# Kernel tuning notes

Hardware: AMD Instinct MI355X
Metric: run time of the kernel (lower is better)

## Reference

```python
import jax, jax.numpy as jnp
import numpy as np

N_NODES = 100000
N_EDGES = 1600000
D = 128
L = 4          # GIN layers
H = 32         # inner MLP hidden width (hard-coded in create_mlp)
BN_EPS = 1e-5


def setup_inputs() -> dict:
    key = jax.random.key(0)
    ks = jax.random.split(key, 8)
    X = jax.random.normal(ks[0], (N_NODES, D), dtype=jnp.float32)
    edge_index = jax.random.randint(ks[1], (2, N_EDGES), 0, N_NODES, dtype=jnp.int64)
    eps = jax.random.normal(ks[2], (L,), dtype=jnp.float32)
    W1 = jax.random.normal(ks[3], (L, H, D), dtype=jnp.float32) * 0.1
    W2 = jax.random.normal(ks[4], (L, H, H), dtype=jnp.float32) * 0.1
    W3 = jax.random.normal(ks[5], (L, D, H), dtype=jnp.float32) * 0.1
    return {
        "X": X, "edge_index": edge_index, "eps": eps,
        "W1": W1, "b1": jnp.zeros((L, H), jnp.float32),
        "g1": jnp.ones((L, H), jnp.float32), "bt1": jnp.zeros((L, H), jnp.float32),
        "W2": W2, "b2": jnp.zeros((L, H), jnp.float32),
        "g2": jnp.ones((L, H), jnp.float32), "bt2": jnp.zeros((L, H), jnp.float32),
        "W3": W3, "b3": jnp.zeros((L, D), jnp.float32),
    }


def _bn(x, g, b):
    # BatchNorm1d in training mode: biased batch stats over the node axis
    m = jnp.mean(x, axis=0)
    v = jnp.var(x, axis=0)
    return g * (x - m) * jax.lax.rsqrt(v + BN_EPS) + b


def reference(X, edge_index, eps, W1, b1, g1, bt1, W2, b2, g2, bt2, W3, b3):
    src, dst = edge_index[0], edge_index[1]
    for l in range(L):
        # identity-message scatter-add neighbor aggregation
        S = jax.ops.segment_sum(X[src], dst, num_segments=N_NODES)  # [N, D_l]
        Z = (1.0 + eps[l]) * X + S
        # inner MLP: Lin->BN->ReLU, Lin->BN->ReLU, Lin
        h = jax.nn.relu(_bn(Z @ W1[l].T + b1[l], g1[l], bt1[l]))
        h = jax.nn.relu(_bn(h @ W2[l].T + b2[l], g2[l], bt2[l]))
        X = h @ W3[l].T + b3[l]
    return X
```

## Files before the change

### kernel.cpp

```cpp
#include <hip/hip_runtime.h>

#define NN 100000
#define NE 1600000
#define DD 128
#define HH 32
#define NB 196
#define SB 256
#define EPB 6250
#define BCAP 12288

#define OFF_P        0UL
#define OFF_T        12800000UL
#define OFF_PK       25600000UL
#define OFF_ROWOFF   32000000UL
#define OFF_COUNTS   32400128UL
#define OFF_POFS     32600832UL
#define OFF_BTOT     32801536UL
#define OFF_BBASE    32802560UL
#define OFF_STATS    32803584UL
#define OFF_W1T      32819968UL
#define OFF_W2T      32836352UL
#define OFF_MT       32852736UL
#define OFF_C        32865024UL
#define OFF_W3T      32865536UL

__global__ void __launch_bounds__(256) k_count(const int* __restrict__ ei,
                                               int* __restrict__ counts) {
    __shared__ int c[NB];
    int t = threadIdx.x;
    if (t < NB) c[t] = 0;
    __syncthreads();
    int s = blockIdx.x * EPB;
    for (int e = s + t; e < s + EPB; e += 256)
        atomicAdd(&c[ei[NE + e] >> 9], 1);
    __syncthreads();
    if (t < NB) counts[t * SB + blockIdx.x] = c[t];
}

__global__ void __launch_bounds__(256) k_scanX(const int* __restrict__ counts,
                                               int* __restrict__ pofs,
                                               int* __restrict__ btot) {
    __shared__ int s[256];
    int t = threadIdx.x, b = blockIdx.x;
    int v = counts[b * SB + t];
    s[t] = v;
    __syncthreads();
    for (int off = 1; off < 256; off <<= 1) {
        int x = (t >= off) ? s[t - off] : 0;
        __syncthreads();
        s[t] += x;
        __syncthreads();
    }
    pofs[b * SB + t] = s[t] - v;
    if (t == 255) btot[b] = s[255];
}

__global__ void __launch_bounds__(256) k_scanY(const int* __restrict__ btot,
                                               int* __restrict__ bbase,
                                               int* __restrict__ row_off) {
    __shared__ int s[256];
    int t = threadIdx.x;
    int v = (t < NB) ? btot[t] : 0;
    s[t] = v;
    __syncthreads();
    for (int off = 1; off < 256; off <<= 1) {
        int x = (t >= off) ? s[t - off] : 0;
        __syncthreads();
        s[t] += x;
        __syncthreads();
    }
    if (t < NB) bbase[t] = s[t] - v;
    if (t == NB - 1) bbase[NB] = s[t];
    if (t == 0) row_off[NN] = NE;
}

__global__ void __launch_bounds__(256) k_scatter(const int* __restrict__ ei,
                                                 const int* __restrict__ pofs,
                                                 const int* __restrict__ bbase,
                                                 int* __restrict__ pk) {
    __shared__ int cur[NB];
    int t = threadIdx.x, blk = blockIdx.x;
    if (t < NB) cur[t] = bbase[t] + pofs[t * SB + blk];
    __syncthreads();
    int s = blk * EPB;
    for (int e = s + t; e < s + EPB; e += 256) {
        int src = ei[e], dst = ei[NE + e];
        int b = dst >> 9;
        int pos = atomicAdd(&cur[b], 1);
        pk[pos] = (src << 9) | (dst & 511);
    }
}

__global__ void __launch_bounds__(256) k_bucket(int* pk,
                                                const int* __restrict__ bbase,
                                                int* __restrict__ row_off) {
    __shared__ int cnt[512];
    __shared__ int ts[256];
    __shared__ int stage[BCAP];
    int t = threadIdx.x, b = blockIdx.x;
    int base = bbase[b], end = bbase[b + 1];
    cnt[t] = 0; cnt[t + 256] = 0;
    __syncthreads();
    for (int e = base + t; e < end; e += 256)
        atomicAdd(&cnt[pk[e] & 511], 1);
    __syncthreads();
    int a0 = cnt[2 * t], a1 = cnt[2 * t + 1];
    int p = a0 + a1;
    ts[t] = p;
    __syncthreads();
    for (int off = 1; off < 256; off <<= 1) {
        int x = (t >= off) ? ts[t - off] : 0;
        __syncthreads();
        ts[t] += x;
        __syncthreads();
    }
    int ex = ts[t] - p;
    cnt[2 * t] = ex;
    cnt[2 * t + 1] = ex + a0;
    int n0 = b * 512 + 2 * t;
    if (n0 < NN)     row_off[n0]     = base + ex;
    if (n0 + 1 < NN) row_off[n0 + 1] = base + ex + a0;
    __syncthreads();
    for (int e = base + t; e < end; e += 256) {
        int v = pk[e];
        int pos = atomicAdd(&cnt[v & 511], 1);
        stage[pos] = v >> 9;
    }
    __syncthreads();
    int sz = end - base;
    for (int i = t; i < sz; i += 256) pk[base + i] = stage[i];
}

__global__ void __launch_bounds__(256) k_prep(const float* __restrict__ W1,
                                              const float* __restrict__ W2,
                                              const float* __restrict__ W3,
                                              const float* __restrict__ b3,
                                              float* __restrict__ W1T,
                                              float* __restrict__ W2T,
                                              float* __restrict__ MT,
                                              float* __restrict__ C,
                                              float* __restrict__ W3T) {
    int t = threadIdx.x, b = blockIdx.x;
    if (b < 12) {
        int d = b * 256 + t;
        int l = d >> 10, rem = d & 1023;
        int i = rem >> 5, j = rem & 31;
        const float* w1r = W1 + (l + 1) * HH * DD + i * DD;
        const float* w3c = W3 + l * DD * HH + j;
        float m = 0.f;
#pragma unroll 8
        for (int k = 0; k < DD; k++) m += w1r[k] * w3c[k * HH];
        MT[l * 1024 + j * 32 + i] = m;
    } else if (b == 12) {
        for (int idx = t; idx < 4096; idx += 256) {
            int jj = idx >> 7, kk = idx & 127;
            W1T[kk * 32 + jj] = W1[jj * 128 + kk];
        }
    } else if (b == 13) {
        for (int idx = t; idx < 4096; idx += 256) {
            int l = idx >> 10, rem = idx & 1023;
            int i = rem >> 5, j = rem & 31;
            W2T[l * 1024 + j * 32 + i] = W2[l * 1024 + i * 32 + j];
        }
    } else if (b == 14) {
        for (int idx = t; idx < 4096; idx += 256) {
            int jj = idx >> 5, kk = idx & 31;
            W3T[kk * 128 + jj] = W3[3 * 4096 + jj * 32 + kk];
        }
    } else {
        if (t < 96) {
            int l = t >> 5, ii = t & 31;
            const float* w1r = W1 + (l + 1) * HH * DD + ii * DD;
            const float* bb = b3 + l * DD;
            float c = 0.f;
#pragma unroll 8
            for (int k = 0; k < DD; k++) c += w1r[k] * bb[k];
            C[l * 32 + ii] = c;
        }
    }
}

__global__ void __launch_bounds__(256) k_P(const float4* __restrict__ X4,
                                           const float4* __restrict__ W1T4,
                                           float4* __restrict__ P4) {
    __shared__ float xs[128 * 33];
    int t = threadIdx.x, blk = blockIdx.x;
    int i = t & 7, g = t >> 3;
    int nbase = blk * 128;
    float4 acc[4];
#pragma unroll
    for (int j = 0; j < 4; j++) acc[j] = make_float4(0.f, 0.f, 0.f, 0.f);
    for (int kt = 0; kt < 4; kt++) {
        __syncthreads();
#pragma unroll
        for (int q = 0; q < 4; q++) {
            int idx = t + 256 * q;
            int nd = idx >> 3, c4 = idx & 7;
            int node = nbase + nd;
            if (node > NN - 1) node = NN - 1;
            float4 v = X4[(size_t)node * 32 + kt * 8 + c4];
            float* dst = xs + nd * 33 + 4 * c4;
            dst[0] = v.x; dst[1] = v.y; dst[2] = v.z; dst[3] = v.w;
        }
        __syncthreads();
        const float4* Wk = W1T4 + (size_t)(kt * 32) * 8 + i;
        const float* xr0 = xs + (g * 4) * 33;
#pragma unroll
        for (int k = 0; k < 32; k++) {
            float4 w = Wk[k * 8];
            float x0 = xr0[k], x1 = xr0[33 + k], x2 = xr0[66 + k], x3 = xr0[99 + k];
            acc[0].x += x0 * w.x; acc[0].y += x0 * w.y; acc[0].z += x0 * w.z; acc[0].w += x0 * w.w;
            acc[1].x += x1 * w.x; acc[1].y += x1 * w.y; acc[1].z += x1 * w.z; acc[1].w += x1 * w.w;
            acc[2].x += x2 * w.x; acc[2].y += x2 * w.y; acc[2].z += x2 * w.z; acc[2].w += x2 * w.w;
            acc[3].x += x3 * w.x; acc[3].y += x3 * w.y; acc[3].z += x3 * w.z; acc[3].w += x3 * w.w;
        }
    }
    int node = nbase + g * 4;
#pragma unroll
    for (int j = 0; j < 4; j++)
        if (node + j < NN) P4[(size_t)(node + j) * 8 + i] = acc[j];
}

__global__ void __launch_bounds__(256) k_A(const float4* __restrict__ P4,
                                           const int* __restrict__ csr,
                                           const int* __restrict__ row_off,
                                           const float* __restrict__ eps,
                                           const float* __restrict__ b1, int l,
                                           float4* __restrict__ T4,
                                           float* __restrict__ gs) {
    __shared__ float ls[64];
    int t = threadIdx.x;
    if (t < 64) ls[t] = 0.f;
    __syncthreads();
    int g = t >> 3, i = t & 7;
    int n = blockIdx.x * 32 + g;
    float e1 = 1.f + eps[l];
    int e0 = row_off[n], eend = row_off[n + 1];
    float4 p = P4[(size_t)n * 8 + i];
    float4 acc;
    acc.x = e1 * p.x; acc.y = e1 * p.y; acc.z = e1 * p.z; acc.w = e1 * p.w;
    int e = e0;
    for (; e + 4 <= eend; e += 4) {
        int s0 = csr[e], s1 = csr[e + 1], s2 = csr[e + 2], s3 = csr[e + 3];
        float4 q0 = P4[(size_t)s0 * 8 + i];
        float4 q1 = P4[(size_t)s1 * 8 + i];
        float4 q2 = P4[(size_t)s2 * 8 + i];
        float4 q3 = P4[(size_t)s3 * 8 + i];
        acc.x += (q0.x + q1.x) + (q2.x + q3.x);
        acc.y += (q0.y + q1.y) + (q2.y + q3.y);
        acc.z += (q0.z + q1.z) + (q2.z + q3.z);
        acc.w += (q0.w + q1.w) + (q2.w + q3.w);
    }
    for (; e < eend; e++) {
        int s = csr[e];
        float4 q = P4[(size_t)s * 8 + i];
        acc.x += q.x; acc.y += q.y; acc.z += q.z; acc.w += q.w;
    }
    float4 bb = ((const float4*)(b1 + l * 32))[i];
    acc.x += bb.x; acc.y += bb.y; acc.z += bb.z; acc.w += bb.w;
    T4[(size_t)n * 8 + i] = acc;
    float sx = acc.x, sy = acc.y, sz = acc.z, sw = acc.w;
    float qx = acc.x * acc.x, qy = acc.y * acc.y, qz = acc.z * acc.z, qw = acc.w * acc.w;
#pragma unroll
    for (int off = 8; off < 64; off <<= 1) {
        sx += __shfl_xor(sx, off); sy += __shfl_xor(sy, off);
        sz += __shfl_xor(sz, off); sw += __shfl_xor(sw, off);
        qx += __shfl_xor(qx, off); qy += __shfl_xor(qy, off);
        qz += __shfl_xor(qz, off); qw += __shfl_xor(qw, off);
    }
    if ((t & 56) == 0) {
        atomicAdd(&ls[4 * i + 0], sx); atomicAdd(&ls[4 * i + 1], sy);
        atomicAdd(&ls[4 * i + 2], sz); atomicAdd(&ls[4 * i + 3], sw);
        atomicAdd(&ls[32 + 4 * i + 0], qx); atomicAdd(&ls[32 + 4 * i + 1], qy);
        atomicAdd(&ls[32 + 4 * i + 2], qz); atomicAdd(&ls[32 + 4 * i + 3], qw);
    }
    __syncthreads();
    if (t < 64) atomicAdd(&gs[(blockIdx.x & 7) * 64 + t], ls[t]);
}

__global__ void __launch_bounds__(256) k_D(float4* __restrict__ T4,
                                           const float4* __restrict__ W2T4,
                                           const float* __restrict__ b2,
                                           const float* __restrict__ g1,
                                           const float* __restrict__ bt1, int l,
                                           float* __restrict__ gs) {
    __shared__ float sc[32], sh[32], ls[64], a1s[128 * 33];
    int t = threadIdx.x, blk = blockIdx.x;
    if (t < 32) {
        float s0 = 0.f, s1 = 0.f;
#pragma unroll
        for (int r = 0; r < 8; r++) { s0 += gs[r * 64 + t]; s1 += gs[r * 64 + 32 + t]; }
        float m = s0 * (1.f / NN);
        float var = s1 * (1.f / NN) - m * m;
        float s = g1[l * 32 + t] * rsqrtf(var + 1e-5f);
        sc[t] = s; sh[t] = bt1[l * 32 + t] - m * s;
    } else if (t >= 64 && t < 128) {
        ls[t - 64] = 0.f;
    }
    __syncthreads();
    int nbase = blk * 128;
#pragma unroll
    for (int q = 0; q < 4; q++) {
        int idx = t + 256 * q;
        int nd = idx >> 3, c4 = idx & 7;
        int node = nbase + nd;
        if (node > NN - 1) node = NN - 1;
        float4 x = T4[(size_t)node * 8 + c4];
        float* dst = a1s + nd * 33 + 4 * c4;
        dst[0] = fmaxf(x.x * sc[4 * c4 + 0] + sh[4 * c4 + 0], 0.f);
        dst[1] = fmaxf(x.y * sc[4 * c4 + 1] + sh[4 * c4 + 1], 0.f);
        dst[2] = fmaxf(x.z * sc[4 * c4 + 2] + sh[4 * c4 + 2], 0.f);
        dst[3] = fmaxf(x.w * sc[4 * c4 + 3] + sh[4 * c4 + 3], 0.f);
    }
    __syncthreads();
    int i = t & 7, g = t >> 3;
    const float4* b24 = (const float4*)(b2 + l * 32);
    float4 b = b24[i];
    float4 acc[4];
#pragma unroll
    for (int j = 0; j < 4; j++) acc[j] = b;
    const float* xr0 = a1s + (g * 4) * 33;
#pragma unroll
    for (int k = 0; k < 32; k++) {
        float4 w = W2T4[k * 8 + i];
        float x0 = xr0[k], x1 = xr0[33 + k], x2 = xr0[66 + k], x3 = xr0[99 + k];
        acc[0].x += x0 * w.x; acc[0].y += x0 * w.y; acc[0].z += x0 * w.z; acc[0].w += x0 * w.w;
        acc[1].x += x1 * w.x; acc[1].y += x1 * w.y; acc[1].z += x1 * w.z; acc[1].w += x1 * w.w;
        acc[2].x += x2 * w.x; acc[2].y += x2 * w.y; acc[2].z += x2 * w.z; acc[2].w += x2 * w.w;
        acc[3].x += x3 * w.x; acc[3].y += x3 * w.y; acc[3].z += x3 * w.z; acc[3].w += x3 * w.w;
    }
    int node = nbase + g * 4;
    float sx = 0.f, sy = 0.f, sz = 0.f, sw = 0.f;
    float qx = 0.f, qy = 0.f, qz = 0.f, qw = 0.f;
#pragma unroll
    for (int j = 0; j < 4; j++) {
        if (node + j < NN) {
            T4[(size_t)(node + j) * 8 + i] = acc[j];
            sx += acc[j].x; sy += acc[j].y; sz += acc[j].z; sw += acc[j].w;
            qx += acc[j].x * acc[j].x; qy += acc[j].y * acc[j].y;
            qz += acc[j].z * acc[j].z; qw += acc[j].w * acc[j].w;
        }
    }
#pragma unroll
    for (int off = 8; off < 64; off <<= 1) {
        sx += __shfl_xor(sx, off); sy += __shfl_xor(sy, off);
        sz += __shfl_xor(sz, off); sw += __shfl_xor(sw, off);
        qx += __shfl_xor(qx, off); qy += __shfl_xor(qy, off);
        qz += __shfl_xor(qz, off); qw += __shfl_xor(qw, off);
    }
    if ((t & 56) == 0) {
        atomicAdd(&ls[4 * i + 0], sx); atomicAdd(&ls[4 * i + 1], sy);
        atomicAdd(&ls[4 * i + 2], sz); atomicAdd(&ls[4 * i + 3], sw);
        atomicAdd(&ls[32 + 4 * i + 0], qx); atomicAdd(&ls[32 + 4 * i + 1], qy);
        atomicAdd(&ls[32 + 4 * i + 2], qz); atomicAdd(&ls[32 + 4 * i + 3], qw);
    }
    __syncthreads();
    if (t < 64) atomicAdd(&gs[512 + (blk & 7) * 64 + t], ls[t]);
}

__global__ void __launch_bounds__(256) k_Fm(const float4* __restrict__ T4,
                                            const float* __restrict__ g2,
                                            const float* __restrict__ bt2, int l,
                                            const float* __restrict__ gs,
                                            const float4* __restrict__ MT4,
                                            const float* __restrict__ C,
                                            float4* __restrict__ P4) {
    __shared__ float sc[32], sh[32], a2s[128 * 33];
    int t = threadIdx.x, blk = blockIdx.x;
    if (t < 32) {
        float s0 = 0.f, s1 = 0.f;
#pragma unroll
        for (int r = 0; r < 8; r++) { s0 += gs[512 + r * 64 + t]; s1 += gs[512 + r * 64 + 32 + t]; }
        float m = s0 * (1.f / NN);
        float var = s1 * (1.f / NN) - m * m;
        float s = g2[l * 32 + t] * rsqrtf(var + 1e-5f);
        sc[t] = s; sh[t] = bt2[l * 32 + t] - m * s;
    }
    __syncthreads();
    int nbase = blk * 128;
#pragma unroll
    for (int q = 0; q < 4; q++) {
        int idx = t + 256 * q;
        int nd = idx >> 3, c4 = idx & 7;
        int node = nbase + nd;
        if (node > NN - 1) node = NN - 1;
        float4 x = T4[(size_t)node * 8 + c4];
        float* dst = a2s + nd * 33 + 4 * c4;
        dst[0] = fmaxf(x.x * sc[4 * c4 + 0] + sh[4 * c4 + 0], 0.f);
        dst[1] = fmaxf(x.y * sc[4 * c4 + 1] + sh[4 * c4 + 1], 0.f);
        dst[2] = fmaxf(x.z * sc[4 * c4 + 2] + sh[4 * c4 + 2], 0.f);
        dst[3] = fmaxf(x.w * sc[4 * c4 + 3] + sh[4 * c4 + 3], 0.f);
    }
    __syncthreads();
    int i = t & 7, g = t >> 3;
    const float4* C4 = (const float4*)(C + l * 32);
    float4 c0 = C4[i];
    float4 acc[4];
#pragma unroll
    for (int j = 0; j < 4; j++) acc[j] = c0;
    const float* xr0 = a2s + (g * 4) * 33;
    const float4* Mt = MT4 + l * 256;
#pragma unroll
    for (int k = 0; k < 32; k++) {
        float4 w = Mt[k * 8 + i];
        float x0 = xr0[k], x1 = xr0[33 + k], x2 = xr0[66 + k], x3 = xr0[99 + k];
        acc[0].x += x0 * w.x; acc[0].y += x0 * w.y; acc[0].z += x0 * w.z; acc[0].w += x0 * w.w;
        acc[1].x += x1 * w.x; acc[1].y += x1 * w.y; acc[1].z += x1 * w.z; acc[1].w += x1 * w.w;
        acc[2].x += x2 * w.x; acc[2].y += x2 * w.y; acc[2].z += x2 * w.z; acc[2].w += x2 * w.w;
        acc[3].x += x3 * w.x; acc[3].y += x3 * w.y; acc[3].z += x3 * w.z; acc[3].w += x3 * w.w;
    }
    int node = nbase + g * 4;
#pragma unroll
    for (int j = 0; j < 4; j++)
        if (node + j < NN) P4[(size_t)(node + j) * 8 + i] = acc[j];
}

__global__ void __launch_bounds__(256) k_F3(const float4* __restrict__ T4,
                                            const float* __restrict__ g2,
                                            const float* __restrict__ bt2,
                                            const float* __restrict__ gs,
                                            const float4* __restrict__ W3T4,
                                            const float* __restrict__ b3,
                                            float4* __restrict__ out4) {
    __shared__ float sc[32], sh[32], a2s[32 * 33];
    int t = threadIdx.x, blk = blockIdx.x;
    if (t < 32) {
        float s0 = 0.f, s1 = 0.f;
#pragma unroll
        for (int r = 0; r < 8; r++) { s0 += gs[512 + r * 64 + t]; s1 += gs[512 + r * 64 + 32 + t]; }
        float m = s0 * (1.f / NN);
        float var = s1 * (1.f / NN) - m * m;
        float s = g2[3 * 32 + t] * rsqrtf(var + 1e-5f);
        sc[t] = s; sh[t] = bt2[3 * 32 + t] - m * s;
    }
    __syncthreads();
    {
        int nd = t >> 3, c4 = t & 7;
        float4 x = T4[(size_t)(blk * 32 + nd) * 8 + c4];
        float* dst = a2s + nd * 33 + 4 * c4;
        dst[0] = fmaxf(x.x * sc[4 * c4 + 0] + sh[4 * c4 + 0], 0.f);
        dst[1] = fmaxf(x.y * sc[4 * c4 + 1] + sh[4 * c4 + 1], 0.f);
        dst[2] = fmaxf(x.z * sc[4 * c4 + 2] + sh[4 * c4 + 2], 0.f);
        dst[3] = fmaxf(x.w * sc[4 * c4 + 3] + sh[4 * c4 + 3], 0.f);
    }
    __syncthreads();
    int j = t & 31, g = t >> 5;
    const float4* b34 = (const float4*)(b3 + 3 * 128);
    float4 b = b34[j];
    float4 acc[4];
#pragma unroll
    for (int jj = 0; jj < 4; jj++) acc[jj] = b;
    const float* xr0 = a2s + (g * 4) * 33;
#pragma unroll
    for (int k = 0; k < 32; k++) {
        float4 w = W3T4[k * 32 + j];
        float x0 = xr0[k], x1 = xr0[33 + k], x2 = xr0[66 + k], x3 = xr0[99 + k];
        acc[0].x += x0 * w.x; acc[0].y += x0 * w.y; acc[0].z += x0 * w.z; acc[0].w += x0 * w.w;
        acc[1].x += x1 * w.x; acc[1].y += x1 * w.y; acc[1].z += x1 * w.z; acc[1].w += x1 * w.w;
        acc[2].x += x2 * w.x; acc[2].y += x2 * w.y; acc[2].z += x2 * w.z; acc[2].w += x2 * w.w;
        acc[3].x += x3 * w.x; acc[3].y += x3 * w.y; acc[3].z += x3 * w.z; acc[3].w += x3 * w.w;
    }
    size_t node = (size_t)blk * 32 + g * 4;
#pragma unroll
    for (int jj = 0; jj < 4; jj++)
        out4[(node + jj) * 32 + j] = acc[jj];
}

extern "C" void kernel_launch(void* const* d_in, const int* in_sizes, int n_in,
                              void* d_out, int out_size, void* d_ws, size_t ws_size,
                              hipStream_t stream) {
    const float* X   = (const float*)d_in[0];
    const int*   EI  = (const int*)d_in[1];
    const float* eps = (const float*)d_in[2];
    const float* W1  = (const float*)d_in[3];
    const float* b1  = (const float*)d_in[4];
    const float* g1  = (const float*)d_in[5];
    const float* bt1 = (const float*)d_in[6];
    const float* W2  = (const float*)d_in[7];
    const float* b2  = (const float*)d_in[8];
    const float* g2  = (const float*)d_in[9];
    const float* bt2 = (const float*)d_in[10];
    const float* W3  = (const float*)d_in[11];
    const float* b3  = (const float*)d_in[12];

    char* ws = (char*)d_ws;
    float* P       = (float*)(ws + OFF_P);
    float* T       = (float*)(ws + OFF_T);
    int*   pk      = (int*)(ws + OFF_PK);
    int*   row_off = (int*)(ws + OFF_ROWOFF);
    int*   counts  = (int*)(ws + OFF_COUNTS);
    int*   pofs    = (int*)(ws + OFF_POFS);
    int*   btot    = (int*)(ws + OFF_BTOT);
    int*   bbase   = (int*)(ws + OFF_BBASE);
    float* stats   = (float*)(ws + OFF_STATS);
    float* W1T     = (float*)(ws + OFF_W1T);
    float* W2T     = (float*)(ws + OFF_W2T);
    float* MT      = (float*)(ws + OFF_MT);
    float* C       = (float*)(ws + OFF_C);
    float* W3T     = (float*)(ws + OFF_W3T);

    hipMemsetAsync(ws + OFF_STATS, 0, 16384, stream);

    k_count<<<SB, 256, 0, stream>>>(EI, counts);
    k_prep<<<16, 256, 0, stream>>>(W1, W2, W3, b3, W1T, W2T, MT, C, W3T);
    k_scanX<<<NB, 256, 0, stream>>>(counts, pofs, btot);
    k_scanY<<<1, 256, 0, stream>>>(btot, bbase, row_off);
    k_scatter<<<SB, 256, 0, stream>>>(EI, pofs, bbase, pk);
    k_bucket<<<NB, 256, 0, stream>>>(pk, bbase, row_off);
    k_P<<<782, 256, 0, stream>>>((const float4*)X, (const float4*)W1T, (float4*)P);

    for (int l = 0; l < 4; l++) {
        float* gs = stats + l * 1024;
        k_A<<<NN / 32, 256, 0, stream>>>((const float4*)P, pk, row_off, eps, b1, l,
                                         (float4*)T, gs);
        k_D<<<782, 256, 0, stream>>>((float4*)T,
                                     (const float4*)(W2T + (size_t)l * 1024),
                                     b2, g1, bt1, l, gs);
        if (l < 3)
            k_Fm<<<782, 256, 0, stream>>>((const float4*)T, g2, bt2, l, gs,
                                          (const float4*)MT, C, (float4*)P);
        else
            k_F3<<<3125, 256, 0, stream>>>((const float4*)T, g2, bt2, gs,
                                           (const float4*)W3T, b3, (float4*)d_out);
    }
}
```

Before: 475.2 us.

## Partition CSR edges by source quarter and gather per quarter for locality

Each node's incoming edges are now sorted into four source-index ranges, with a 4×N offset table replacing row_off. The aggregation kernel has each block handle 128 nodes and walks the quarters in sequence, so gathers from all blocks running at once tend to hit the same 3.2 MB slice of P and stay in cache. The costs are fewer, larger blocks with more registers each, a bigger offset table, and more histogram bins in the bucket kernel.

After: 554.0 us. +16.6%, slower.

```diff
diff --git a/kernel.cpp b/kernel.cpp
--- a/kernel.cpp
+++ b/kernel.cpp
@@ -8,21 +8,26 @@
 #define SB 256
 #define EPB 6250
 #define BCAP 12288
+#define QS 25000
 
 #define OFF_P        0UL
 #define OFF_T        12800000UL
 #define OFF_PK       25600000UL
-#define OFF_ROWOFF   32000000UL
-#define OFF_COUNTS   32400128UL
-#define OFF_POFS     32600832UL
-#define OFF_BTOT     32801536UL
-#define OFF_BBASE    32802560UL
-#define OFF_STATS    32803584UL
-#define OFF_W1T      32819968UL
-#define OFF_W2T      32836352UL
-#define OFF_MT       32852736UL
-#define OFF_C        32865024UL
-#define OFF_W3T      32865536UL
+#define OFF_QOFF     32000000UL
+#define OFF_COUNTS   33600128UL
+#define OFF_POFS     33800832UL
+#define OFF_BTOT     34001536UL
+#define OFF_BBASE    34002560UL
+#define OFF_STATS    34003584UL
+#define OFF_W1T      34019968UL
+#define OFF_W2T      34036352UL
+#define OFF_MT       34052736UL
+#define OFF_C        34065024UL
+#define OFF_W3T      34065536UL
+
+__device__ __forceinline__ int src_quad(int s) {
+    return (s >= 2 * QS) ? ((s >= 3 * QS) ? 3 : 2) : ((s >= QS) ? 1 : 0);
+}
 
 __global__ void __launch_bounds__(256) k_count(const int* __restrict__ ei,
                                                int* __restrict__ counts) {
@@ -57,7 +62,7 @@
 
 __global__ void __launch_bounds__(256) k_scanY(const int* __restrict__ btot,
                                                int* __restrict__ bbase,
-                                               int* __restrict__ row_off) {
+                                               int* __restrict__ qoff) {
     __shared__ int s[256];
     int t = threadIdx.x;
     int v = (t < NB) ? btot[t] : 0;
@@ -71,7 +76,7 @@
     }
     if (t < NB) bbase[t] = s[t] - v;
     if (t == NB - 1) bbase[NB] = s[t];
-    if (t == 0) row_off[NN] = NE;
+    if (t == 0) qoff[4 * NN] = NE;
 }
 
 __global__ void __launch_bounds__(256) k_scatter(const int* __restrict__ ei,
@@ -93,19 +98,24 @@
 
 __global__ void __launch_bounds__(256) k_bucket(int* pk,
                                                 const int* __restrict__ bbase,
-                                                int* __restrict__ row_off) {
-    __shared__ int cnt[512];
+                                                int* __restrict__ qoff) {
+    __shared__ int cnt[2048];
     __shared__ int ts[256];
     __shared__ int stage[BCAP];
     int t = threadIdx.x, b = blockIdx.x;
     int base = bbase[b], end = bbase[b + 1];
-    cnt[t] = 0; cnt[t + 256] = 0;
-    __syncthreads();
-    for (int e = base + t; e < end; e += 256)
-        atomicAdd(&cnt[pk[e] & 511], 1);
-    __syncthreads();
-    int a0 = cnt[2 * t], a1 = cnt[2 * t + 1];
-    int p = a0 + a1;
+#pragma unroll
+    for (int j = 0; j < 8; j++) cnt[t * 8 + j] = 0;
+    __syncthreads();
+    for (int e = base + t; e < end; e += 256) {
+        int v = pk[e];
+        atomicAdd(&cnt[((v & 511) << 2) | src_quad(v >> 9)], 1);
+    }
+    __syncthreads();
+    int c8[8];
+    int p = 0;
+#pragma unroll
+    for (int j = 0; j < 8; j++) { c8[j] = cnt[t * 8 + j]; p += c8[j]; }
     ts[t] = p;
     __syncthreads();
     for (int off = 1; off < 256; off <<= 1) {
@@ -114,17 +124,21 @@
         ts[t] += x;
         __syncthreads();
     }
-    int ex = ts[t] - p;
-    cnt[2 * t] = ex;
-    cnt[2 * t + 1] = ex + a0;
-    int n0 = b * 512 + 2 * t;
-    if (n0 < NN)     row_off[n0]     = base + ex;
-    if (n0 + 1 < NN) row_off[n0 + 1] = base + ex + a0;
+    int run = ts[t] - p;
+#pragma unroll
+    for (int j = 0; j < 8; j++) {
+        int ci = t * 8 + j;
+        cnt[ci] = run;
+        int n0 = b * 512 + (ci >> 2);
+        if (n0 < NN) qoff[n0 * 4 + (ci & 3)] = base + run;
+        run += c8[j];
+    }
     __syncthreads();
     for (int e = base + t; e < end; e += 256) {
         int v = pk[e];
-        int pos = atomicAdd(&cnt[v & 511], 1);
-        stage[pos] = v >> 9;
+        int src = v >> 9;
+        int pos = atomicAdd(&cnt[((v & 511) << 2) | src_quad(src)], 1);
+        stage[pos] = src;
     }
     __syncthreads();
     int sz = end - base;
@@ -223,7 +237,7 @@
 
 __global__ void __launch_bounds__(256) k_A(const float4* __restrict__ P4,
                                            const int* __restrict__ csr,
-                                           const int* __restrict__ row_off,
+                                           const int* __restrict__ qoff,
                                            const float* __restrict__ eps,
                                            const float* __restrict__ b1, int l,
                                            float4* __restrict__ T4,
@@ -231,36 +245,60 @@
     __shared__ float ls[64];
     int t = threadIdx.x;
     if (t < 64) ls[t] = 0.f;
-    __syncthreads();
     int g = t >> 3, i = t & 7;
-    int n = blockIdx.x * 32 + g;
+    int nbase = blockIdx.x * 128;
     float e1 = 1.f + eps[l];
-    int e0 = row_off[n], eend = row_off[n + 1];
-    float4 p = P4[(size_t)n * 8 + i];
-    float4 acc;
-    acc.x = e1 * p.x; acc.y = e1 * p.y; acc.z = e1 * p.z; acc.w = e1 * p.w;
-    int e = e0;
-    for (; e + 4 <= eend; e += 4) {
-        int s0 = csr[e], s1 = csr[e + 1], s2 = csr[e + 2], s3 = csr[e + 3];
-        float4 q0 = P4[(size_t)s0 * 8 + i];
-        float4 q1 = P4[(size_t)s1 * 8 + i];
-        float4 q2 = P4[(size_t)s2 * 8 + i];
-        float4 q3 = P4[(size_t)s3 * 8 + i];
-        acc.x += (q0.x + q1.x) + (q2.x + q3.x);
-        acc.y += (q0.y + q1.y) + (q2.y + q3.y);
-        acc.z += (q0.z + q1.z) + (q2.z + q3.z);
-        acc.w += (q0.w + q1.w) + (q2.w + q3.w);
-    }
-    for (; e < eend; e++) {
-        int s = csr[e];
-        float4 q = P4[(size_t)s * 8 + i];
-        acc.x += q.x; acc.y += q.y; acc.z += q.z; acc.w += q.w;
+    float4 acc[4];
+#pragma unroll
+    for (int p = 0; p < 4; p++) {
+        int n = nbase + p * 32 + g;
+        if (n < NN) {
+            float4 x = P4[(size_t)n * 8 + i];
+            acc[p].x = e1 * x.x; acc[p].y = e1 * x.y;
+            acc[p].z = e1 * x.z; acc[p].w = e1 * x.w;
+        } else {
+            acc[p] = make_float4(0.f, 0.f, 0.f, 0.f);
+        }
+    }
+#pragma unroll 1
+    for (int q = 0; q < 4; q++) {
+#pragma unroll
+        for (int p = 0; p < 4; p++) {
+            int n = nbase + p * 32 + g;
+            if (n >= NN) continue;
+            int e = qoff[4 * n + q], ee = qoff[4 * n + q + 1];
+            for (; e + 4 <= ee; e += 4) {
+                int s0 = csr[e], s1 = csr[e + 1], s2 = csr[e + 2], s3 = csr[e + 3];
+                float4 q0 = P4[(size_t)s0 * 8 + i];
+                float4 q1 = P4[(size_t)s1 * 8 + i];
+                float4 q2 = P4[(size_t)s2 * 8 + i];
+                float4 q3 = P4[(size_t)s3 * 8 + i];
+                acc[p].x += (q0.x + q1.x) + (q2.x + q3.x);
+                acc[p].y += (q0.y + q1.y) + (q2.y + q3.y);
+                acc[p].z += (q0.z + q1.z) + (q2.z + q3.z);
+                acc[p].w += (q0.w + q1.w) + (q2.w + q3.w);
+            }
+            for (; e < ee; e++) {
+                int s = csr[e];
+                float4 qv = P4[(size_t)s * 8 + i];
+                acc[p].x += qv.x; acc[p].y += qv.y; acc[p].z += qv.z; acc[p].w += qv.w;
+            }
+        }
     }
     float4 bb = ((const float4*)(b1 + l * 32))[i];
-    acc.x += bb.x; acc.y += bb.y; acc.z += bb.z; acc.w += bb.w;
-    T4[(size_t)n * 8 + i] = acc;
-    float sx = acc.x, sy = acc.y, sz = acc.z, sw = acc.w;
-    float qx = acc.x * acc.x, qy = acc.y * acc.y, qz = acc.z * acc.z, qw = acc.w * acc.w;
+    float sx = 0.f, sy = 0.f, sz = 0.f, sw = 0.f;
+    float qx = 0.f, qy = 0.f, qz = 0.f, qw = 0.f;
+#pragma unroll
+    for (int p = 0; p < 4; p++) {
+        int n = nbase + p * 32 + g;
+        if (n < NN) {
+            acc[p].x += bb.x; acc[p].y += bb.y; acc[p].z += bb.z; acc[p].w += bb.w;
+            T4[(size_t)n * 8 + i] = acc[p];
+            sx += acc[p].x; sy += acc[p].y; sz += acc[p].z; sw += acc[p].w;
+            qx += acc[p].x * acc[p].x; qy += acc[p].y * acc[p].y;
+            qz += acc[p].z * acc[p].z; qw += acc[p].w * acc[p].w;
+        }
+    }
 #pragma unroll
     for (int off = 8; off < 64; off <<= 1) {
         sx += __shfl_xor(sx, off); sy += __shfl_xor(sy, off);
@@ -268,6 +306,7 @@
         qx += __shfl_xor(qx, off); qy += __shfl_xor(qy, off);
         qz += __shfl_xor(qz, off); qw += __shfl_xor(qw, off);
     }
+    __syncthreads();
     if ((t & 56) == 0) {
         atomicAdd(&ls[4 * i + 0], sx); atomicAdd(&ls[4 * i + 1], sy);
         atomicAdd(&ls[4 * i + 2], sz); atomicAdd(&ls[4 * i + 3], sw);
@@ -487,7 +526,7 @@
     float* P       = (float*)(ws + OFF_P);
     float* T       = (float*)(ws + OFF_T);
     int*   pk      = (int*)(ws + OFF_PK);
-    int*   row_off = (int*)(ws + OFF_ROWOFF);
+    int*   qoff    = (int*)(ws + OFF_QOFF);
     int*   counts  = (int*)(ws + OFF_COUNTS);
     int*   pofs    = (int*)(ws + OFF_POFS);
     int*   btot    = (int*)(ws + OFF_BTOT);
@@ -504,15 +543,15 @@
     k_count<<<SB, 256, 0, stream>>>(EI, counts);
     k_prep<<<16, 256, 0, stream>>>(W1, W2, W3, b3, W1T, W2T, MT, C, W3T);
     k_scanX<<<NB, 256, 0, stream>>>(counts, pofs, btot);
-    k_scanY<<<1, 256, 0, stream>>>(btot, bbase, row_off);
+    k_scanY<<<1, 256, 0, stream>>>(btot, bbase, qoff);
     k_scatter<<<SB, 256, 0, stream>>>(EI, pofs, bbase, pk);
-    k_bucket<<<NB, 256, 0, stream>>>(pk, bbase, row_off);
+    k_bucket<<<NB, 256, 0, stream>>>(pk, bbase, qoff);
     k_P<<<782, 256, 0, stream>>>((const float4*)X, (const float4*)W1T, (float4*)P);
 
     for (int l = 0; l < 4; l++) {
         float* gs = stats + l * 1024;
-        k_A<<<NN / 32, 256, 0, stream>>>((const float4*)P, pk, row_off, eps, b1, l,
-                                         (float4*)T, gs);
+        k_A<<<782, 256, 0, stream>>>((const float4*)P, pk, qoff, eps, b1, l,
+                                     (float4*)T, gs);
         k_D<<<782, 256, 0, stream>>>((float4*)T,
                                      (const float4*)(W2T + (size_t)l * 1024),
                                      b2, g1, bt1, l, gs);
```
